# Optimization experiments

Hardware: AMD Instinct MI355X
Metric: run time of the kernel (lower is better)

## Reference

```python
import jax, jax.numpy as jnp
import numpy as np

IN_FEATURES = 4096
OUT_FEATURES = 11008
INTERLEAVE = 4
KSTRIDE = 64

# Inverse of the per-32-column AWQ shuffle applied in pack_int4_weight.
# Forward shuffle (on a length-32 index vector):
#   step1: reshape(4,4,2).transpose(1,0,2)  (swap axes 2,3 of [N,Kg,4,4,2])
#   step2: reshape(4,4,2).transpose(0,2,1)  (swap last two axes)
_a = np.arange(32)
_s1 = _a.reshape(4, 4, 2).transpose(1, 0, 2).reshape(32)
_s2p = _a.reshape(4, 4, 2).transpose(0, 2, 1).reshape(32)
_PERM32 = _s1[_s2p]            # shuffled[i] = orig[_PERM32[i]]
INV32 = np.argsort(_PERM32)     # orig[j] = shuffled[INV32[j]]


def setup_inputs() -> dict:
    key = jax.random.key(0)
    k1, k2, k3, k4, k5 = jax.random.split(key, 5)
    x = jax.random.normal(k1, (64, IN_FEATURES), dtype=jnp.float32)
    # Packed int4 weights: [N//interleave, K]; random 16-bit words unpack to
    # random int4 quant codes in [0, 15].
    qweight = jax.random.randint(
        k2, (OUT_FEATURES // INTERLEAVE, IN_FEATURES), 0, 65536, dtype=jnp.int32)
    scale = jax.random.uniform(k3, (OUT_FEATURES, 1), dtype=jnp.float32) * 0.01 + 1e-4
    zero_point = jax.random.uniform(k4, (OUT_FEATURES, 1), dtype=jnp.float32) * 15.0
    bias = jax.random.normal(k5, (OUT_FEATURES,), dtype=jnp.float32)
    return {"x": x, "qweight": qweight, "scale": scale,
            "zero_point": zero_point, "bias": bias}


def _unpack_int4(qweight):
    """Inverse of pack_int4_weight: [N//4, K] packed words -> [N, K] int4 codes."""
    Nq, K = qweight.shape
    N = Nq * INTERLEAVE
    p = qweight.astype(jnp.int32)
    # split nibbles: last axis is the interleave dim of the pack
    nib = jnp.stack([(p >> (4 * i)) & 0xF for i in range(INTERLEAVE)], axis=-1)  # [Nq, K, 4]
    # invert: [Nq, Kg, kstride, interleave] -> [Nq, Kg, interleave, kstride]
    nib = nib.reshape(Nq, K // KSTRIDE, KSTRIDE, INTERLEAVE)
    nib = nib.reshape(Nq, K // KSTRIDE, INTERLEAVE, KSTRIDE)
    # invert transpose(0,2,1,3) that moved interleave inside
    nib = nib.transpose(0, 2, 1, 3).reshape(N, K)
    # invert the per-32-column shuffle
    q = nib.reshape(N, K // 32, 32)[..., jnp.asarray(INV32)].reshape(N, K)
    return q


def reference(x, qweight, scale, zero_point, bias):
    q = _unpack_int4(qweight)
    q = jnp.clip(q, 0, 15).astype(jnp.float32)          # asymmetric 4-bit codes
    w = (q - zero_point) * scale                         # [N, K] dequantized weight
    return x @ w.T + bias                                # F.linear(x, w, bias)
```

## Files before the change

### kernel.cpp

```cpp
#include <hip/hip_runtime.h>
#include <hip/hip_bf16.h>

#define K_DIM 4096
#define N_DIM 11008

typedef __attribute__((ext_vector_type(4))) float f32x4;
typedef _Float16 half8 __attribute__((ext_vector_type(8)));
typedef _Float16 half2v __attribute__((ext_vector_type(2)));
typedef unsigned int uint32;

__global__ __launch_bounds__(256) void prep_x(const float* __restrict__ x,
                                              unsigned short* __restrict__ xp) {
    const int g = blockIdx.x * 256 + threadIdx.x;
    const int lane = g & 63, mt = (g >> 6) & 3, h = (g >> 8) & 1, kg = g >> 9;
    const int m = mt * 16 + (lane & 15), qq = lane >> 4;
    union { unsigned short v[8]; uint4 u4; } r;
#pragma unroll
    for (int e = 0; e < 8; ++e) {
        const int kp = h * 32 + qq * 8 + e;
        const int t = kp >> 2, ip = kp & 3;
        const int i = ((ip & 1) << 1) | (ip >> 1);
        const int col = ((t >> 3) << 5) + (t & 7) + (i << 3);
        const _Float16 hf = (_Float16)x[m * K_DIM + kg * 64 + col];
        r.v[e] = __builtin_bit_cast(unsigned short, hf);
    }
    *(uint4*)(xp + (size_t)g * 8) = r.u4;
}

__device__ __forceinline__ half8 build_bfrag(int w0, int w1, half2v s2, half2v c2) {
    union { half8 h; half2v p[4]; } r;
    const half2v k1024 = {(_Float16)1024.0f, (_Float16)1024.0f};
    const uint32 u0 = (uint32)(w0 & 0xF)        | (((uint32)w0 & 0xF00u) << 8) | 0x64006400u;
    const uint32 u1 = (uint32)((w0 >> 4) & 0xF) | (((uint32)w0 & 0xF000u) << 4) | 0x64006400u;
    const uint32 u2 = (uint32)(w1 & 0xF)        | (((uint32)w1 & 0xF00u) << 8) | 0x64006400u;
    const uint32 u3 = (uint32)((w1 >> 4) & 0xF) | (((uint32)w1 & 0xF000u) << 4) | 0x64006400u;
    half2v q;
    q = __builtin_bit_cast(half2v, u0) - k1024; r.p[0] = q * s2 + c2;
    q = __builtin_bit_cast(half2v, u1) - k1024; r.p[1] = q * s2 + c2;
    q = __builtin_bit_cast(half2v, u2) - k1024; r.p[2] = q * s2 + c2;
    q = __builtin_bit_cast(half2v, u3) - k1024; r.p[3] = q * s2 + c2;
    return r.h;
}

__global__ __launch_bounds__(256) void w4_gemm(
    const unsigned short* __restrict__ xp,
    const int*   __restrict__ qw,
    const float* __restrict__ scale,
    const float* __restrict__ zp,
    const float* __restrict__ bias,
    float*       __restrict__ out)
{
    __shared__ f32x4 part[1024];

    const int tid = threadIdx.x, lane = tid & 63, j = tid >> 6;
    const int nl = lane & 15, q = lane >> 4;
    const int n0 = blockIdx.x * 16, nn = n0 + nl;

    const float s = scale[nn], z = zp[nn];
    const _Float16 sh = (_Float16)s;
    const _Float16 ch = (_Float16)(-z * s);
    const half2v s2 = {sh, sh}, c2 = {ch, ch};

    const int* qb = qw + ((size_t)(nn >> 2) * K_DIM) + ((nn & 3) * 16) + 2 * q;

    f32x4 acc[4] = {{0,0,0,0},{0,0,0,0},{0,0,0,0},{0,0,0,0}};

    const int kg_end = j * 16 + 16;
    for (int kg = j * 16; kg < kg_end; ++kg) {
        const int2 wA = *(const int2*)(qb + kg * 64);
        const int2 wB = *(const int2*)(qb + kg * 64 + 8);
        const unsigned short* ab = xp + (size_t)kg * 4096;

        half8 bf = build_bfrag(wA.x, wA.y, s2, c2);
#pragma unroll
        for (int mt = 0; mt < 4; ++mt) {
            const half8 af = *(const half8*)(ab + mt * 512 + lane * 8);
            acc[mt] = __builtin_amdgcn_mfma_f32_16x16x32_f16(af, bf, acc[mt], 0, 0, 0);
        }
        bf = build_bfrag(wB.x, wB.y, s2, c2);
#pragma unroll
        for (int mt = 0; mt < 4; ++mt) {
            const half8 af = *(const half8*)(ab + (4 + mt) * 512 + lane * 8);
            acc[mt] = __builtin_amdgcn_mfma_f32_16x16x32_f16(af, bf, acc[mt], 0, 0, 0);
        }
    }

#pragma unroll
    for (int mt = 0; mt < 4; ++mt)
        part[(j * 16 + mt * 4 + q) * 16 + nl] = acc[mt];
    __syncthreads();

    {
        const int rmt = tid >> 6, rq = (tid >> 4) & 3, rnl = tid & 15;
        const int base = rmt * 64 + rq * 16 + rnl;
        f32x4 sum = part[base];
        sum += part[256 + base];
        sum += part[512 + base];
        sum += part[768 + base];
        const float bv = bias[n0 + rnl];
        const int m0 = rmt * 16 + rq * 4;
#pragma unroll
        for (int r = 0; r < 4; ++r)
            out[(size_t)(m0 + r) * N_DIM + n0 + rnl] = sum[r] + bv;
    }
}

extern "C" void kernel_launch(void* const* d_in, const int* in_sizes, int n_in,
                              void* d_out, int out_size, void* d_ws, size_t ws_size,
                              hipStream_t stream) {
    const float* x     = (const float*)d_in[0];
    const int*   qw    = (const int*)d_in[1];
    const float* scale = (const float*)d_in[2];
    const float* zp    = (const float*)d_in[3];
    const float* bias  = (const float*)d_in[4];
    float* out = (float*)d_out;
    unsigned short* xp = (unsigned short*)d_ws;

    prep_x<<<128, 256, 0, stream>>>(x, xp);
    w4_gemm<<<N_DIM / 16, 256, 0, stream>>>(xp, qw, scale, zp, bias, out);
}
```

Baseline: 33.50 us.

## Split K across blocks with 32-column tiles and add a separate reduction kernel

```diff
diff --git a/kernel.cpp b/kernel.cpp
--- a/kernel.cpp
+++ b/kernel.cpp
@@ -47,61 +47,96 @@
     const int*   __restrict__ qw,
     const float* __restrict__ scale,
     const float* __restrict__ zp,
-    const float* __restrict__ bias,
-    float*       __restrict__ out)
+    f32x4*       __restrict__ ws)
 {
-    __shared__ f32x4 part[1024];
+    __shared__ f32x4 part[2048];
 
     const int tid = threadIdx.x, lane = tid & 63, j = tid >> 6;
     const int nl = lane & 15, q = lane >> 4;
-    const int n0 = blockIdx.x * 16, nn = n0 + nl;
+    const int nx = blockIdx.x, ky = blockIdx.y;
+    const int n0 = nx * 32;
+    const int nnA = n0 + nl, nnB = n0 + 16 + nl;
 
-    const float s = scale[nn], z = zp[nn];
-    const _Float16 sh = (_Float16)s;
-    const _Float16 ch = (_Float16)(-z * s);
-    const half2v s2 = {sh, sh}, c2 = {ch, ch};
+    const float sA = scale[nnA], zA = zp[nnA];
+    const float sB = scale[nnB], zB = zp[nnB];
+    const _Float16 shA = (_Float16)sA, chA = (_Float16)(-zA * sA);
+    const _Float16 shB = (_Float16)sB, chB = (_Float16)(-zB * sB);
+    const half2v s2A = {shA, shA}, c2A = {chA, chA};
+    const half2v s2B = {shB, shB}, c2B = {chB, chB};
 
-    const int* qb = qw + ((size_t)(nn >> 2) * K_DIM) + ((nn & 3) * 16) + 2 * q;
+    const int* qbA = qw + ((size_t)(nnA >> 2) * K_DIM) + ((nnA & 3) * 16) + 2 * q;
+    const int* qbB = qw + ((size_t)(nnB >> 2) * K_DIM) + ((nnB & 3) * 16) + 2 * q;
 
-    f32x4 acc[4] = {{0,0,0,0},{0,0,0,0},{0,0,0,0},{0,0,0,0}};
+    f32x4 acc[2][4] = {};
 
-    const int kg_end = j * 16 + 16;
-    for (int kg = j * 16; kg < kg_end; ++kg) {
-        const int2 wA = *(const int2*)(qb + kg * 64);
-        const int2 wB = *(const int2*)(qb + kg * 64 + 8);
+    const int kg0 = ky * 16 + j * 4;
+#pragma unroll
+    for (int it = 0; it < 4; ++it) {
+        const int kg = kg0 + it;
+        const int2 a0 = *(const int2*)(qbA + kg * 64);
+        const int2 a1 = *(const int2*)(qbA + kg * 64 + 8);
+        const int2 b0 = *(const int2*)(qbB + kg * 64);
+        const int2 b1 = *(const int2*)(qbB + kg * 64 + 8);
         const unsigned short* ab = xp + (size_t)kg * 4096;
 
-        half8 bf = build_bfrag(wA.x, wA.y, s2, c2);
+        const half8 bfA0 = build_bfrag(a0.x, a0.y, s2A, c2A);
+        const half8 bfB0 = build_bfrag(b0.x, b0.y, s2B, c2B);
 #pragma unroll
         for (int mt = 0; mt < 4; ++mt) {
             const half8 af = *(const half8*)(ab + mt * 512 + lane * 8);
-            acc[mt] = __builtin_amdgcn_mfma_f32_16x16x32_f16(af, bf, acc[mt], 0, 0, 0);
+            acc[0][mt] = __builtin_amdgcn_mfma_f32_16x16x32_f16(af, bfA0, acc[0][mt], 0, 0, 0);
+            acc[1][mt] = __builtin_amdgcn_mfma_f32_16x16x32_f16(af, bfB0, acc[1][mt], 0, 0, 0);
         }
-        bf = build_bfrag(wB.x, wB.y, s2, c2);
+        const half8 bfA1 = build_bfrag(a1.x, a1.y, s2A, c2A);
+        const half8 bfB1 = build_bfrag(b1.x, b1.y, s2B, c2B);
 #pragma unroll
         for (int mt = 0; mt < 4; ++mt) {
             const half8 af = *(const half8*)(ab + (4 + mt) * 512 + lane * 8);
-            acc[mt] = __builtin_amdgcn_mfma_f32_16x16x32_f16(af, bf, acc[mt], 0, 0, 0);
+            acc[0][mt] = __builtin_amdgcn_mfma_f32_16x16x32_f16(af, bfA1, acc[0][mt], 0, 0, 0);
+            acc[1][mt] = __builtin_amdgcn_mfma_f32_16x16x32_f16(af, bfB1, acc[1][mt], 0, 0, 0);
         }
     }
 
 #pragma unroll
-    for (int mt = 0; mt < 4; ++mt)
-        part[(j * 16 + mt * 4 + q) * 16 + nl] = acc[mt];
+    for (int nt = 0; nt < 2; ++nt)
+#pragma unroll
+        for (int mt = 0; mt < 4; ++mt)
+            part[((j * 2 + nt) * 4 + mt) * 64 + q * 16 + nl] = acc[nt][mt];
     __syncthreads();
 
-    {
-        const int rmt = tid >> 6, rq = (tid >> 4) & 3, rnl = tid & 15;
-        const int base = rmt * 64 + rq * 16 + rnl;
-        f32x4 sum = part[base];
-        sum += part[256 + base];
-        sum += part[512 + base];
-        sum += part[768 + base];
-        const float bv = bias[n0 + rnl];
-        const int m0 = rmt * 16 + rq * 4;
+    f32x4* wsb = ws + ((size_t)nx * 4 + ky) * 512;
+#pragma unroll
+    for (int ss = 0; ss < 2; ++ss) {
+        const int s = tid + ss * 256;
+        f32x4 v = part[s];
+        v += part[512 + s];
+        v += part[1024 + s];
+        v += part[1536 + s];
+        wsb[s] = v;
+    }
+}
+
+__global__ __launch_bounds__(256) void reduce_k(
+    const f32x4* __restrict__ ws,
+    const float* __restrict__ bias,
+    float*       __restrict__ out)
+{
+    const int nx = blockIdx.x, tid = threadIdx.x;
+    const f32x4* wsb = ws + (size_t)nx * 4 * 512;
+#pragma unroll
+    for (int ss = 0; ss < 2; ++ss) {
+        const int s = tid + ss * 256;
+        f32x4 v = wsb[s];
+        v += wsb[512 + s];
+        v += wsb[1024 + s];
+        v += wsb[1536 + s];
+        const int nt = s >> 8, mt = (s >> 6) & 3, qq = (s >> 4) & 3, nl = s & 15;
+        const int n = nx * 32 + nt * 16 + nl;
+        const float bv = bias[n];
+        const int m0 = mt * 16 + qq * 4;
 #pragma unroll
         for (int r = 0; r < 4; ++r)
-            out[(size_t)(m0 + r) * N_DIM + n0 + rnl] = sum[r] + bv;
+            out[(size_t)(m0 + r) * N_DIM + n] = v[r] + bv;
     }
 }
 
@@ -114,8 +149,12 @@
     const float* zp    = (const float*)d_in[3];
     const float* bias  = (const float*)d_in[4];
     float* out = (float*)d_out;
+
     unsigned short* xp = (unsigned short*)d_ws;
+    f32x4* part_ws = (f32x4*)((char*)d_ws + (1 << 20));
 
     prep_x<<<128, 256, 0, stream>>>(x, xp);
-    w4_gemm<<<N_DIM / 16, 256, 0, stream>>>(xp, qw, scale, zp, bias, out);
+    dim3 grid(344, 4);
+    w4_gemm<<<grid, 256, 0, stream>>>(xp, qw, scale, zp, part_ws);
+    reduce_k<<<344, 256, 0, stream>>>(part_ws, bias, out);
 }
```

Result: faster. 30.05 us (-10.3%).

## Share x tiles across waves via LDS double-buffering and split-K with separate reduce

Applied to the files above, without the earlier changes.

```diff
diff --git a/kernel.cpp b/kernel.cpp
--- a/kernel.cpp
+++ b/kernel.cpp
@@ -7,7 +7,10 @@
 typedef __attribute__((ext_vector_type(4))) float f32x4;
 typedef _Float16 half8 __attribute__((ext_vector_type(8)));
 typedef _Float16 half2v __attribute__((ext_vector_type(2)));
+typedef int int2v __attribute__((ext_vector_type(2)));
 typedef unsigned int uint32;
+typedef __attribute__((address_space(1))) const char gchar_t;
+typedef __attribute__((address_space(3))) char lchar_t;
 
 __global__ __launch_bounds__(256) void prep_x(const float* __restrict__ x,
                                               unsigned short* __restrict__ xp) {
@@ -47,61 +50,97 @@
     const int*   __restrict__ qw,
     const float* __restrict__ scale,
     const float* __restrict__ zp,
+    f32x4*       __restrict__ ws)
+{
+    __shared__ alignas(16) char lds[2 * 8192];
+
+    const int tid = threadIdx.x, lane = tid & 63, w = tid >> 6;
+    const int nl = lane & 15, q = lane >> 4;
+    const int nx = blockIdx.x, ky = blockIdx.y;
+    const int n0 = nx * 64;
+    const int kgbase = ky * 8;
+
+    const int nn = n0 + w * 16 + nl;
+    const float sc = scale[nn], z = zp[nn];
+    const _Float16 sh = (_Float16)sc, ch = (_Float16)(-z * sc);
+    const half2v s2 = {sh, sh}, c2 = {ch, ch};
+
+    const int* qb = qw + ((size_t)(nn >> 2) * K_DIM) + ((nn & 3) * 16) + 2 * q
+                       + (size_t)kgbase * 64;
+
+    const char* xp_b = (const char*)xp;
+
+    f32x4 acc[4] = {};
+    int2v qa[2][2];
+
+    {
+        const char* asrc = xp_b + (size_t)kgbase * 8192 + w * 2048 + lane * 16;
+        __builtin_amdgcn_global_load_lds((gchar_t*)asrc,
+                                         (lchar_t*)(&lds[w * 2048]), 16, 0, 0);
+        __builtin_amdgcn_global_load_lds((gchar_t*)(asrc + 1024),
+                                         (lchar_t*)(&lds[w * 2048 + 1024]), 16, 0, 0);
+        qa[0][0] = *(const int2v*)(qb);
+        qa[0][1] = *(const int2v*)(qb + 8);
+    }
+
+#pragma unroll
+    for (int kg = 0; kg < 8; ++kg) {
+        const int slot = kg & 1;
+        asm volatile("s_waitcnt vmcnt(0) lgkmcnt(0)" ::: "memory");
+        __builtin_amdgcn_s_barrier();
+        __builtin_amdgcn_sched_barrier(0);
+
+        if (kg < 7) {
+            const char* asrc = xp_b + (size_t)(kgbase + kg + 1) * 8192
+                             + w * 2048 + lane * 16;
+            char* sb = &lds[(slot ^ 1) * 8192];
+            __builtin_amdgcn_global_load_lds((gchar_t*)asrc,
+                                             (lchar_t*)(sb + w * 2048), 16, 0, 0);
+            __builtin_amdgcn_global_load_lds((gchar_t*)(asrc + 1024),
+                                             (lchar_t*)(sb + w * 2048 + 1024), 16, 0, 0);
+            qa[(kg + 1) & 1][0] = *(const int2v*)(qb + (kg + 1) * 64);
+            qa[(kg + 1) & 1][1] = *(const int2v*)(qb + (kg + 1) * 64 + 8);
+        }
+
+        const char* sb = &lds[slot * 8192];
+#pragma unroll
+        for (int h = 0; h < 2; ++h) {
+            const half8 bf = build_bfrag(qa[kg & 1][h].x, qa[kg & 1][h].y, s2, c2);
+#pragma unroll
+            for (int mt = 0; mt < 4; ++mt) {
+                const half8 af = *(const half8*)(sb + (h * 4 + mt) * 1024 + lane * 16);
+                acc[mt] = __builtin_amdgcn_mfma_f32_16x16x32_f16(af, bf, acc[mt], 0, 0, 0);
+            }
+        }
+    }
+
+    f32x4* wsb = ws + ((size_t)nx * 8 + ky) * 1024;
+#pragma unroll
+    for (int mt = 0; mt < 4; ++mt)
+        wsb[w * 256 + mt * 64 + lane] = acc[mt];
+}
+
+__global__ __launch_bounds__(256) void reduce_k(
+    const f32x4* __restrict__ ws,
     const float* __restrict__ bias,
     float*       __restrict__ out)
 {
-    __shared__ f32x4 part[1024];
-
-    const int tid = threadIdx.x, lane = tid & 63, j = tid >> 6;
-    const int nl = lane & 15, q = lane >> 4;
-    const int n0 = blockIdx.x * 16, nn = n0 + nl;
-
-    const float s = scale[nn], z = zp[nn];
-    const _Float16 sh = (_Float16)s;
-    const _Float16 ch = (_Float16)(-z * s);
-    const half2v s2 = {sh, sh}, c2 = {ch, ch};
-
-    const int* qb = qw + ((size_t)(nn >> 2) * K_DIM) + ((nn & 3) * 16) + 2 * q;
-
-    f32x4 acc[4] = {{0,0,0,0},{0,0,0,0},{0,0,0,0},{0,0,0,0}};
-
-    const int kg_end = j * 16 + 16;
-    for (int kg = j * 16; kg < kg_end; ++kg) {
-        const int2 wA = *(const int2*)(qb + kg * 64);
-        const int2 wB = *(const int2*)(qb + kg * 64 + 8);
-        const unsigned short* ab = xp + (size_t)kg * 4096;
-
-        half8 bf = build_bfrag(wA.x, wA.y, s2, c2);
+    const int nx = blockIdx.x, tid = threadIdx.x;
+    const f32x4* wsb = ws + (size_t)nx * 8192;
 #pragma unroll
-        for (int mt = 0; mt < 4; ++mt) {
-            const half8 af = *(const half8*)(ab + mt * 512 + lane * 8);
-            acc[mt] = __builtin_amdgcn_mfma_f32_16x16x32_f16(af, bf, acc[mt], 0, 0, 0);
-        }
-        bf = build_bfrag(wB.x, wB.y, s2, c2);
+    for (int ss = 0; ss < 4; ++ss) {
+        const int u = tid + ss * 256;
+        f32x4 v = wsb[u];
 #pragma unroll
-        for (int mt = 0; mt < 4; ++mt) {
-            const half8 af = *(const half8*)(ab + (4 + mt) * 512 + lane * 8);
-            acc[mt] = __builtin_amdgcn_mfma_f32_16x16x32_f16(af, bf, acc[mt], 0, 0, 0);
-        }
-    }
-
-#pragma unroll
-    for (int mt = 0; mt < 4; ++mt)
-        part[(j * 16 + mt * 4 + q) * 16 + nl] = acc[mt];
-    __syncthreads();
-
-    {
-        const int rmt = tid >> 6, rq = (tid >> 4) & 3, rnl = tid & 15;
-        const int base = rmt * 64 + rq * 16 + rnl;
-        f32x4 sum = part[base];
-        sum += part[256 + base];
-        sum += part[512 + base];
-        sum += part[768 + base];
-        const float bv = bias[n0 + rnl];
-        const int m0 = rmt * 16 + rq * 4;
+        for (int i = 1; i < 8; ++i)
+            v += wsb[i * 1024 + u];
+        const int w = u >> 8, mt = (u >> 6) & 3, lane = u & 63;
+        const int n = nx * 64 + w * 16 + (lane & 15);
+        const float bv = bias[n];
+        const int m0 = mt * 16 + (lane >> 4) * 4;
 #pragma unroll
         for (int r = 0; r < 4; ++r)
-            out[(size_t)(m0 + r) * N_DIM + n0 + rnl] = sum[r] + bv;
+            out[(size_t)(m0 + r) * N_DIM + n] = v[r] + bv;
     }
 }
 
@@ -114,8 +153,12 @@
     const float* zp    = (const float*)d_in[3];
     const float* bias  = (const float*)d_in[4];
     float* out = (float*)d_out;
+
     unsigned short* xp = (unsigned short*)d_ws;
+    f32x4* part_ws = (f32x4*)((char*)d_ws + (1 << 20));
 
     prep_x<<<128, 256, 0, stream>>>(x, xp);
-    w4_gemm<<<N_DIM / 16, 256, 0, stream>>>(xp, qw, scale, zp, bias, out);
+    dim3 grid(172, 8);
+    w4_gemm<<<grid, 256, 0, stream>>>(xp, qw, scale, zp, part_ws);
+    reduce_k<<<172, 256, 0, stream>>>(part_ws, bias, out);
 }
```

Result: faster. 29.91 us (-10.7%).
